# Optimization experiments

Hardware: AMD Instinct MI355X
Metric: run time of the kernel (lower is better)

Reference implementation:

```python
import jax, jax.numpy as jnp
import numpy as np

N, E, IN, HID, OUT, H, G = 50000, 800000, 128, 32, 32, 4, 64
NEG_SLOPE = 0.2


def setup_inputs() -> dict:
    key = jax.random.key(0)
    ks = jax.random.split(key, 12)
    p = lambda k, s: jax.random.normal(k, s, jnp.float32) * 0.1
    x = jax.random.normal(ks[0], (N, IN), jnp.float32)
    edge_index = jax.random.randint(ks[1], (2, E), 0, N, dtype=jnp.int64)
    batch = jnp.sort(jax.random.randint(ks[2], (N,), 0, G, dtype=jnp.int64))
    return {
        'x': x, 'edge_index': edge_index, 'batch': batch,
        'W1': p(ks[3], (IN, H * HID)),
        'att_src1': p(ks[4], (H, HID)), 'att_dst1': p(ks[5], (H, HID)),
        'b1': jnp.zeros((H * HID,), jnp.float32),
        'W2': p(ks[6], (H * HID, H * OUT)),
        'att_src2': p(ks[7], (H, OUT)), 'att_dst2': p(ks[8], (H, OUT)),
        'b2': jnp.zeros((H * OUT,), jnp.float32),
        'lin_w': p(ks[9], (H * OUT, 1)),
        'lin_b': jnp.zeros((1,), jnp.float32),
    }


def gat_conv(x, src, dst, W, a_src, a_dst, b, heads, ch):
    # x: [N, F_in]; src/dst: [E'] with self-loops already appended.
    n = x.shape[0]
    h = (x @ W).reshape(n, heads, ch)                      # [N, H, C]
    alpha_s = jnp.einsum('nhc,hc->nh', h, a_src)           # [N, H]
    alpha_d = jnp.einsum('nhc,hc->nh', h, a_dst)
    e = jax.nn.leaky_relu(alpha_s[src] + alpha_d[dst], NEG_SLOPE)  # [E', H]
    # segment softmax over destination neighborhoods
    m = jax.ops.segment_max(e, dst, num_segments=n)
    m = jnp.where(jnp.isfinite(m), m, 0.0)
    ex = jnp.exp(e - m[dst])
    s = jax.ops.segment_sum(ex, dst, num_segments=n)
    alpha = ex / (s[dst] + 1e-16)                          # [E', H]
    out = jax.ops.segment_sum(alpha[:, :, None] * h[src], dst, num_segments=n)
    return out.reshape(n, heads * ch) + b


def reference(x, edge_index, batch, W1, att_src1, att_dst1, b1,
              W2, att_src2, att_dst2, b2, lin_w, lin_b):
    # add self-loops (PyG GATConv default add_self_loops=True)
    loops = jnp.arange(N, dtype=edge_index.dtype)
    src = jnp.concatenate([edge_index[0], loops])
    dst = jnp.concatenate([edge_index[1], loops])

    h = jax.nn.elu(gat_conv(x, src, dst, W1, att_src1, att_dst1, b1, H, HID))
    h = gat_conv(h, src, dst, W2, att_src2, att_dst2, b2, H, OUT)  # [N, H*OUT]

    # global mean + max pool per graph
    counts = jax.ops.segment_sum(jnp.ones((N,), h.dtype), batch, num_segments=G)
    mean_p = jax.ops.segment_sum(h, batch, num_segments=G) / jnp.maximum(counts, 1.0)[:, None]
    max_p = jax.ops.segment_max(h, batch, num_segments=G)
    max_p = jnp.where(jnp.isfinite(max_p), max_p, 0.0)
    pooled = mean_p + max_p                                # [G, H*OUT]
    return pooled @ lin_w + lin_b                          # [G, 1]
```

## Files before the change

kernel.cpp:

```cpp
#include <hip/hip_runtime.h>
#include <hip/hip_bf16.h>
#include <hip/hip_fp16.h>
#include <math.h>

#define NEG_SLOPE 0.2f
#define BCAP 64
#define LAYER_W 18432

typedef _Float16 half8 __attribute__((ext_vector_type(8)));
typedef _Float16 half4v __attribute__((ext_vector_type(4)));
typedef float f32x4 __attribute__((ext_vector_type(4)));


__device__ __forceinline__ int lbound(const int* __restrict__ a, int n, int key) {
    int lo = 0, hi = n;
    while (lo < hi) {
        int mid = (lo + hi) >> 1;
        if (a[mid] < key) lo = mid + 1; else hi = mid;
    }
    return lo;
}

__device__ __forceinline__ unsigned encf(float f) {
    unsigned u = __float_as_uint(f);
    return (u & 0x80000000u) ? ~u : (u | 0x80000000u);
}
__device__ __forceinline__ float decf(unsigned u) {
    return (u & 0x80000000u) ? __uint_as_float(u & 0x7FFFFFFFu) : __uint_as_float(~u);
}


__global__ void prep_kernel(const float* __restrict__ W1, const float* __restrict__ W2,
                            const float* __restrict__ as1, const float* __restrict__ ad1,
                            const float* __restrict__ as2, const float* __restrict__ ad2,
                            _Float16* __restrict__ wt_hi, _Float16* __restrict__ wt_lo,
                            int* __restrict__ cnt, float* __restrict__ gsum,
                            unsigned* __restrict__ gmax, int n, int gtot) {
    int b = blockIdx.x;
    if (b < 72) {
        int lane = threadIdx.x;
        if (lane >= 64) return;
        int layer = b / 36;
        int rem = b % 36;
        int nt = rem >> 2;
        int kc = rem & 3;
        const float* W  = layer ? W2 : W1;
        const float* As = layer ? as2 : as1;
        const float* Ad = layer ? ad2 : ad1;
        int nn = lane & 15, q = lane >> 4;
        size_t base = (size_t)layer * LAYER_W + (size_t)((nt * 4 + kc) * 64 + lane) * 8;
        #pragma unroll
        for (int j = 0; j < 8; ++j) {
            int k = kc * 32 + q * 8 + j;
            float w = 0.f;
            if (nt < 8) {
                w = W[(size_t)k * 128 + nt * 16 + nn];
            } else if (nn < 4) {
                for (int c = 0; c < 32; ++c) w += W[(size_t)k * 128 + nn * 32 + c] * As[nn * 32 + c];
            } else if (nn < 8) {
                int hh = nn - 4;
                for (int c = 0; c < 32; ++c) w += W[(size_t)k * 128 + hh * 32 + c] * Ad[hh * 32 + c];
            }
            _Float16 hi = (_Float16)w;
            wt_hi[base + j] = hi;
            wt_lo[base + j] = (_Float16)(w - (float)hi);
        }
        return;
    }
    int i = (b - 72) * 256 + threadIdx.x;
    if (i < n) cnt[i] = 0;
    if (i < gtot) { gsum[i] = 0.f; gmax[i] = 0u; }
}


__global__ void build_kernel(const int* __restrict__ src, const int* __restrict__ dst,
                             int* __restrict__ cnt, unsigned short* __restrict__ col,
                             int E, int n) {
    int part  = blockIdx.x & 7;
    int chunk = blockIdx.x >> 3;
    int i = chunk * 256 + threadIdx.x;
    if (i >= E) return;
    int d = dst[i];
    int psz = (n + 7) >> 3;
    int lo = part * psz;
    if (d < lo || d >= lo + psz) return;
    int slot = atomicAdd(&cnt[d], 1);
    if (slot < BCAP - 1) col[(size_t)d * BCAP + slot] = (unsigned short)src[i];
}


template <bool A16>
__global__ __launch_bounds__(256) void gemm_attn_kernel(
        const void* __restrict__ Araw,
        const _Float16* __restrict__ wt_hi, const _Float16* __restrict__ wt_lo,
        _Float16* __restrict__ H16, float* __restrict__ as_, float* __restrict__ ad_,
        int M) {
    __shared__ _Float16 a_st[64][136];

    int tid = threadIdx.x;
    int m0 = blockIdx.x * 64;

    if (A16) {
        const _Float16* A = (const _Float16*)Araw;
        #pragma unroll
        for (int t = 0; t < 4; ++t) {
            int f = tid + t * 256;
            int r = f >> 4;
            int c8 = (f & 15) << 3;
            int gr = m0 + r; if (gr >= M) gr = M - 1;
            *(half8*)&a_st[r][c8] = *(const half8*)(A + (size_t)gr * 128 + c8);
        }
    } else {
        const float* A = (const float*)Araw;
        #pragma unroll
        for (int t = 0; t < 8; ++t) {
            int f = tid + t * 256;
            int r = f >> 5;
            int c4 = (f & 31) << 2;
            int gr = m0 + r; if (gr >= M) gr = M - 1;
            const float4 v = *(const float4*)(A + (size_t)gr * 128 + c4);
            half4v hi = { (_Float16)v.x, (_Float16)v.y, (_Float16)v.z, (_Float16)v.w };
            *(half4v*)&a_st[r][c4] = hi;
        }
    }
    __syncthreads();

    int w = tid >> 6;
    int lane = tid & 63;
    int cbase = lane & 15;
    int q = lane >> 4;
    int mrow = (w << 4) + cbase;

    f32x4 acc[9];
    #pragma unroll
    for (int nt = 0; nt < 9; ++nt) acc[nt] = (f32x4){0.f, 0.f, 0.f, 0.f};

    #pragma unroll
    for (int kc = 0; kc < 4; ++kc) {
        half8 ah = *(half8*)&a_st[mrow][kc * 32 + q * 8];
        #pragma unroll
        for (int nt = 0; nt < 9; ++nt) {
            const half8 bh = *(const half8*)(wt_hi + (size_t)((nt * 4 + kc) * 64 + lane) * 8);
            const half8 bl = *(const half8*)(wt_lo + (size_t)((nt * 4 + kc) * 64 + lane) * 8);
            acc[nt] = __builtin_amdgcn_mfma_f32_16x16x32_f16(ah, bh, acc[nt], 0, 0, 0);
            acc[nt] = __builtin_amdgcn_mfma_f32_16x16x32_f16(ah, bl, acc[nt], 0, 0, 0);
        }
    }

    #pragma unroll
    for (int nt = 0; nt < 8; ++nt) {
        int c = nt * 16 + cbase;
        #pragma unroll
        for (int i = 0; i < 4; ++i) {
            int gr = m0 + (w << 4) + (q << 2) + i;
            if (gr < M) H16[(size_t)gr * 128 + c] = (_Float16)acc[nt][i];
        }
    }
    if (cbase < 8) {
        #pragma unroll
        for (int i = 0; i < 4; ++i) {
            int gr = m0 + (w << 4) + (q << 2) + i;
            if (gr < M) {
                if (cbase < 4) as_[(size_t)gr * 4 + cbase]     = acc[8][i];
                else           ad_[(size_t)gr * 4 + cbase - 4] = acc[8][i];
            }
        }
    }
}


__global__ __launch_bounds__(256) void agg_kernel(
        const int* __restrict__ cnt, const unsigned short* __restrict__ col,
        const _Float16* __restrict__ h16, const float* __restrict__ as_,
        const float* __restrict__ ad_, const float* __restrict__ bias,
        _Float16* __restrict__ out16, int n, int elu) {
    __shared__ int   s_col[4][64];
    __shared__ float s_w[4][256];

    int wvb  = threadIdx.x >> 6;
    int lane = threadIdx.x & 63;
    int wv   = blockIdx.x * 4 + wvb;
    int valid = (wv < n);
    if (!valid) wv = n - 1;

    int degr = cnt[wv]; if (degr > BCAP - 1) degr = BCAP - 1;
    int deg = degr + 1;
    const unsigned short* crow = col + (size_t)wv * BCAP;
    const float4 adv = *(const float4*)(ad_ + (size_t)wv * 4);

    int q = lane >> 4;
    int r = lane & 15;
    int head = r >> 2;
    const _Float16* hrow = h16 + 8 * r;

    if (lane < deg) {
        int s = (lane == degr) ? wv : (int)crow[lane];
        const float4 av = *(const float4*)(as_ + (size_t)s * 4);
        float e0 = av.x + adv.x, e1 = av.y + adv.y;
        float e2 = av.z + adv.z, e3 = av.w + adv.w;
        float w0 = __expf(fmaxf(e0, NEG_SLOPE * e0));
        float w1 = __expf(fmaxf(e1, NEG_SLOPE * e1));
        float w2 = __expf(fmaxf(e2, NEG_SLOPE * e2));
        float w3 = __expf(fmaxf(e3, NEG_SLOPE * e3));
        s_col[wvb][lane] = s;
        *(float4*)&s_w[wvb][lane * 4] = make_float4(w0, w1, w2, w3);
    } else {
        s_col[wvb][lane] = 0;
        *(float4*)&s_w[wvb][lane * 4] = make_float4(0.f, 0.f, 0.f, 0.f);
    }
    __syncthreads();

    float lsum = 0.f;
    float acc[8];
    #pragma unroll
    for (int j = 0; j < 8; ++j) acc[j] = 0.f;

    for (int it = 0; it < deg; it += 16) {
        int ea = it + q;
        int eb = ea + 4;
        int ec = ea + 8;
        int ed = ea + 12;
        int sa = s_col[wvb][ea];
        int sb = s_col[wvb][eb];
        int sc = s_col[wvb][ec];
        int sd = s_col[wvb][ed];
        float wa = s_w[wvb][ea * 4 + head];
        float wb = s_w[wvb][eb * 4 + head];
        float wc = s_w[wvb][ec * 4 + head];
        float wd = s_w[wvb][ed * 4 + head];
        const half8 ha = *(const half8*)(hrow + (size_t)sa * 128);
        const half8 hb = *(const half8*)(hrow + (size_t)sb * 128);
        const half8 hc = *(const half8*)(hrow + (size_t)sc * 128);
        const half8 hd = *(const half8*)(hrow + (size_t)sd * 128);
        lsum += wa + wb + wc + wd;
        #pragma unroll
        for (int j = 0; j < 8; ++j)
            acc[j] += wa * (float)ha[j] + wb * (float)hb[j]
                    + wc * (float)hc[j] + wd * (float)hd[j];
    }

    #pragma unroll
    for (int j = 0; j < 8; ++j) {
        acc[j] += __shfl_xor(acc[j], 16, 64);
        acc[j] += __shfl_xor(acc[j], 32, 64);
    }
    lsum += __shfl_xor(lsum, 16, 64);
    lsum += __shfl_xor(lsum, 32, 64);

    if (lane < 16 && valid) {
        float inv = 1.f / (lsum + 1e-16f);
        const float4 bv0 = *(const float4*)(bias + 8 * r);
        const float4 bv1 = *(const float4*)(bias + 8 * r + 4);
        float o[8];
        o[0] = acc[0] * inv + bv0.x; o[1] = acc[1] * inv + bv0.y;
        o[2] = acc[2] * inv + bv0.z; o[3] = acc[3] * inv + bv0.w;
        o[4] = acc[4] * inv + bv1.x; o[5] = acc[5] * inv + bv1.y;
        o[6] = acc[6] * inv + bv1.z; o[7] = acc[7] * inv + bv1.w;
        if (elu) {
            #pragma unroll
            for (int j = 0; j < 8; ++j) o[j] = o[j] > 0.f ? o[j] : expm1f(o[j]);
        }
        half8 hv;
        #pragma unroll
        for (int j = 0; j < 8; ++j) hv[j] = (_Float16)o[j];
        *(half8*)(out16 + (size_t)wv * 128 + 8 * r) = hv;
    }
}


__global__ void pool1_kernel(const _Float16* __restrict__ h, const int* __restrict__ batch,
                             float* __restrict__ gsum, unsigned* __restrict__ gmax, int n) {
    int g = blockIdx.x >> 3;
    int p = blockIdx.x & 7;
    int c = threadIdx.x;
    int s = lbound(batch, n, g);
    int e = lbound(batch, n, g + 1);
    int len = e - s;
    int lo = s + (int)((long long)len * p / 8);
    int hi = s + (int)((long long)len * (p + 1) / 8);
    float sum = 0.f, mx = -INFINITY;
    for (int i = lo; i < hi; ++i) {
        float v = (float)h[(size_t)i * 128 + c];
        sum += v; mx = fmaxf(mx, v);
    }
    if (hi > lo) {
        atomicAdd(&gsum[g * 128 + c], sum);
        atomicMax(&gmax[g * 128 + c], encf(mx));
    }
}

__global__ void pool2_kernel(const float* __restrict__ gsum, const unsigned* __restrict__ gmax,
                             const int* __restrict__ batch, const float* __restrict__ lin_w,
                             const float* __restrict__ lin_b, float* __restrict__ out, int n) {
    int g = blockIdx.x;
    int c = threadIdx.x;
    int s = lbound(batch, n, g);
    int e = lbound(batch, n, g + 1);
    float cnt = fmaxf((float)(e - s), 1.0f);
    float mean = gsum[g * 128 + c] / cnt;
    float mx = decf(gmax[g * 128 + c]);
    if (!isfinite(mx)) mx = 0.f;
    float v = (mean + mx) * lin_w[c];
    __shared__ float red[128];
    red[c] = v;
    __syncthreads();
    for (int off = 64; off > 0; off >>= 1) {
        if (c < off) red[c] += red[c + off];
        __syncthreads();
    }
    if (c == 0) out[g] = red[0] + lin_b[0];
}


extern "C" void kernel_launch(void* const* d_in, const int* in_sizes, int n_in,
                              void* d_out, int out_size, void* d_ws, size_t ws_size,
                              hipStream_t stream) {
    const float* x    = (const float*)d_in[0];
    const int*   ei   = (const int*)d_in[1];
    const int*   batch= (const int*)d_in[2];
    const float* W1   = (const float*)d_in[3];
    const float* at_s1= (const float*)d_in[4];
    const float* at_d1= (const float*)d_in[5];
    const float* b1   = (const float*)d_in[6];
    const float* W2   = (const float*)d_in[7];
    const float* at_s2= (const float*)d_in[8];
    const float* at_d2= (const float*)d_in[9];
    const float* b2   = (const float*)d_in[10];
    const float* lw   = (const float*)d_in[11];
    const float* lb   = (const float*)d_in[12];
    float* out = (float*)d_out;

    const int N = in_sizes[0] / 128;
    const int E = in_sizes[1] / 2;
    const int G = out_size;

    char* p = (char*)d_ws;
    auto carve = [&](size_t bytes) -> void* {
        void* q = (void*)p;
        p += (bytes + 255) & ~(size_t)255;
        return q;
    };
    _Float16*       h16   = (_Float16*)carve((size_t)N * 128 * 2);
    _Float16*       a16   = (_Float16*)carve((size_t)N * 128 * 2);
    _Float16*       p16   = (_Float16*)carve((size_t)N * 128 * 2);
    float*          asb   = (float*)carve((size_t)N * 4 * 4);
    float*          adb   = (float*)carve((size_t)N * 4 * 4);
    int*            cnt   = (int*)carve((size_t)N * 4);
    unsigned short* col   = (unsigned short*)carve((size_t)N * BCAP * 2);
    float*          gsum  = (float*)carve((size_t)G * 128 * 4);
    unsigned*       gmax  = (unsigned*)carve((size_t)G * 128 * 4);
    _Float16*       wt_hi = (_Float16*)carve((size_t)2 * LAYER_W * 2);
    _Float16*       wt_lo = (_Float16*)carve((size_t)2 * LAYER_W * 2);

    const int* esrc = ei;
    const int* edst = ei + E;

    int initN = (N > G * 128) ? N : G * 128;
    prep_kernel<<<72 + (initN + 255) / 256, 256, 0, stream>>>(
        W1, W2, at_s1, at_d1, at_s2, at_d2, wt_hi, wt_lo, cnt, gsum, gmax, N, G * 128);

    const int nchunk = (E + 255) / 256;
    build_kernel<<<nchunk * 8, 256, 0, stream>>>(esrc, edst, cnt, col, E, N);

    gemm_attn_kernel<false><<<(N + 63) / 64, 256, 0, stream>>>(
        x, wt_hi, wt_lo, h16, asb, adb, N);
    agg_kernel<<<(N + 3) / 4, 256, 0, stream>>>(
        cnt, col, h16, asb, adb, b1, a16, N, 1);

    gemm_attn_kernel<true><<<(N + 63) / 64, 256, 0, stream>>>(
        a16, wt_hi + LAYER_W, wt_lo + LAYER_W, h16, asb, adb, N);
    agg_kernel<<<(N + 3) / 4, 256, 0, stream>>>(
        cnt, col, h16, asb, adb, b2, p16, N, 0);

    pool1_kernel<<<G * 8, 128, 0, stream>>>(p16, batch, gsum, gmax, N);
    pool2_kernel<<<G, 128, 0, stream>>>(gsum, gmax, batch, lw, lb, out, N);
}
```

Baseline: 280.9 us.

## Software-pipeline neighbor feature gathers in GAT aggregation, drop LDS column staging

The aggregation kernel now reads neighbor column indices straight from global memory as ushort4 per lane group and issues the first half8 feature gathers before the attention-weight computation. Later chunks are double-buffered so each gather overlaps the FMAs of the previous chunk. The shared column array goes away and the block-wide __syncthreads becomes a wave-local lgkmcnt wait, since each wave only reads its own LDS slice. Edge assignment moves from a strided to a contiguous mapping per lane group. Out-of-range slots point at the self row with zero weight, which adds redundant loads but removes the LDS round trip and the barrier.

```diff
diff --git a/kernel.cpp b/kernel.cpp
--- a/kernel.cpp
+++ b/kernel.cpp
@@ -174,7 +174,6 @@
         const _Float16* __restrict__ h16, const float* __restrict__ as_,
         const float* __restrict__ ad_, const float* __restrict__ bias,
         _Float16* __restrict__ out16, int n, int elu) {
-    __shared__ int   s_col[4][64];
     __shared__ float s_w[4][256];
 
     int wvb  = threadIdx.x >> 6;
@@ -186,13 +185,47 @@
     int degr = cnt[wv]; if (degr > BCAP - 1) degr = BCAP - 1;
     int deg = degr + 1;
     const unsigned short* crow = col + (size_t)wv * BCAP;
-    const float4 adv = *(const float4*)(ad_ + (size_t)wv * 4);
 
     int q = lane >> 4;
     int r = lane & 15;
     int head = r >> 2;
     const _Float16* hrow = h16 + 8 * r;
 
+    ushort4 cr0 = *(const ushort4*)(crow + 4 * q);
+    ushort4 cr1 = *(const ushort4*)(crow + 16 + 4 * q);
+
+#define GAT_ISSUE(CR, BASE, H0, H1, H2, H3)                                   \
+    do {                                                                      \
+        int e0_ = (BASE) + 4 * q;                                             \
+        int s0_ = (e0_ + 0 < degr) ? (int)(CR).x : wv;                        \
+        int s1_ = (e0_ + 1 < degr) ? (int)(CR).y : wv;                        \
+        int s2_ = (e0_ + 2 < degr) ? (int)(CR).z : wv;                        \
+        int s3_ = (e0_ + 3 < degr) ? (int)(CR).w : wv;                        \
+        H0 = *(const half8*)(hrow + (size_t)s0_ * 128);                       \
+        H1 = *(const half8*)(hrow + (size_t)s1_ * 128);                       \
+        H2 = *(const half8*)(hrow + (size_t)s2_ * 128);                       \
+        H3 = *(const half8*)(hrow + (size_t)s3_ * 128);                       \
+    } while (0)
+
+#define GAT_FMA(BASE, H0, H1, H2, H3)                                         \
+    do {                                                                      \
+        int e0_ = (BASE) + 4 * q;                                             \
+        float w0_ = s_w[wvb][(e0_ + 0) * 4 + head];                           \
+        float w1_ = s_w[wvb][(e0_ + 1) * 4 + head];                           \
+        float w2_ = s_w[wvb][(e0_ + 2) * 4 + head];                           \
+        float w3_ = s_w[wvb][(e0_ + 3) * 4 + head];                           \
+        lsum += w0_ + w1_ + w2_ + w3_;                                        \
+        _Pragma("unroll")                                                     \
+        for (int j = 0; j < 8; ++j)                                           \
+            acc[j] += w0_ * (float)H0[j] + w1_ * (float)H1[j]                 \
+                    + w2_ * (float)H2[j] + w3_ * (float)H3[j];                \
+    } while (0)
+
+    half8 ha0, ha1, ha2, ha3, hb0, hb1, hb2, hb3;
+
+    GAT_ISSUE(cr0, 0, ha0, ha1, ha2, ha3);
+
+    const float4 adv = *(const float4*)(ad_ + (size_t)wv * 4);
     if (lane < deg) {
         int s = (lane == degr) ? wv : (int)crow[lane];
         const float4 av = *(const float4*)(as_ + (size_t)s * 4);
@@ -202,42 +235,36 @@
         float w1 = __expf(fmaxf(e1, NEG_SLOPE * e1));
         float w2 = __expf(fmaxf(e2, NEG_SLOPE * e2));
         float w3 = __expf(fmaxf(e3, NEG_SLOPE * e3));
-        s_col[wvb][lane] = s;
         *(float4*)&s_w[wvb][lane * 4] = make_float4(w0, w1, w2, w3);
     } else {
-        s_col[wvb][lane] = 0;
         *(float4*)&s_w[wvb][lane * 4] = make_float4(0.f, 0.f, 0.f, 0.f);
     }
-    __syncthreads();
+    asm volatile("s_waitcnt lgkmcnt(0)" ::: "memory");
 
     float lsum = 0.f;
     float acc[8];
     #pragma unroll
     for (int j = 0; j < 8; ++j) acc[j] = 0.f;
 
-    for (int it = 0; it < deg; it += 16) {
-        int ea = it + q;
-        int eb = ea + 4;
-        int ec = ea + 8;
-        int ed = ea + 12;
-        int sa = s_col[wvb][ea];
-        int sb = s_col[wvb][eb];
-        int sc = s_col[wvb][ec];
-        int sd = s_col[wvb][ed];
-        float wa = s_w[wvb][ea * 4 + head];
-        float wb = s_w[wvb][eb * 4 + head];
-        float wc = s_w[wvb][ec * 4 + head];
-        float wd = s_w[wvb][ed * 4 + head];
-        const half8 ha = *(const half8*)(hrow + (size_t)sa * 128);
-        const half8 hb = *(const half8*)(hrow + (size_t)sb * 128);
-        const half8 hc = *(const half8*)(hrow + (size_t)sc * 128);
-        const half8 hd = *(const half8*)(hrow + (size_t)sd * 128);
-        lsum += wa + wb + wc + wd;
-        #pragma unroll
-        for (int j = 0; j < 8; ++j)
-            acc[j] += wa * (float)ha[j] + wb * (float)hb[j]
-                    + wc * (float)hc[j] + wd * (float)hd[j];
-    }
+    if (deg > 16) GAT_ISSUE(cr1, 16, hb0, hb1, hb2, hb3);
+    GAT_FMA(0, ha0, ha1, ha2, ha3);
+    if (deg > 16) {
+        if (deg > 32) {
+            ushort4 cr2 = *(const ushort4*)(crow + 32 + 4 * q);
+            GAT_ISSUE(cr2, 32, ha0, ha1, ha2, ha3);
+        }
+        GAT_FMA(16, hb0, hb1, hb2, hb3);
+        if (deg > 32) {
+            if (deg > 48) {
+                ushort4 cr3 = *(const ushort4*)(crow + 48 + 4 * q);
+                GAT_ISSUE(cr3, 48, hb0, hb1, hb2, hb3);
+            }
+            GAT_FMA(32, ha0, ha1, ha2, ha3);
+            if (deg > 48) GAT_FMA(48, hb0, hb1, hb2, hb3);
+        }
+    }
+#undef GAT_ISSUE
+#undef GAT_FMA
 
     #pragma unroll
     for (int j = 0; j < 8; ++j) {
```

Result: no change. 276.0 us (-1.7%).

## Store self-loops in CSR and prefetch first 32 neighbor rows before softmax

Applied to the files above, without the earlier changes.

Self-loop edges are now written into the neighbor table by the build kernel, and the column buffer is zeroed in the prep kernel. This lets the aggregation kernel issue loads for the first 32 neighbor feature rows right away, before it computes the attention weights, so the exp computation overlaps those gathers. The block-wide barrier is replaced with an lgkmcnt wait, the weight shared-memory layout becomes head-major for vector reads, and a loop over the remaining neighbors handles rare high-degree nodes. The costs are always gathering 32 rows (zero-padded to node 0) even for low-degree nodes, and extra zeroing and build work for the N self-loops.

```diff
diff --git a/kernel.cpp b/kernel.cpp
--- a/kernel.cpp
+++ b/kernel.cpp
@@ -35,7 +35,8 @@
                             const float* __restrict__ as2, const float* __restrict__ ad2,
                             _Float16* __restrict__ wt_hi, _Float16* __restrict__ wt_lo,
                             int* __restrict__ cnt, float* __restrict__ gsum,
-                            unsigned* __restrict__ gmax, int n, int gtot) {
+                            unsigned* __restrict__ gmax, unsigned short* __restrict__ col,
+                            int n, int gtot) {
     int b = blockIdx.x;
     if (b < 72) {
         int lane = threadIdx.x;
@@ -70,6 +71,7 @@
     int i = (b - 72) * 256 + threadIdx.x;
     if (i < n) cnt[i] = 0;
     if (i < gtot) { gsum[i] = 0.f; gmax[i] = 0u; }
+    if (i < n * 8) ((uint4*)col)[i] = make_uint4(0u, 0u, 0u, 0u);
 }
 
 
@@ -79,13 +81,16 @@
     int part  = blockIdx.x & 7;
     int chunk = blockIdx.x >> 3;
     int i = chunk * 256 + threadIdx.x;
-    if (i >= E) return;
-    int d = dst[i];
+    if (i >= E + n) return;
+    int d = (i < E) ? dst[i] : (i - E);
     int psz = (n + 7) >> 3;
     int lo = part * psz;
     if (d < lo || d >= lo + psz) return;
     int slot = atomicAdd(&cnt[d], 1);
-    if (slot < BCAP - 1) col[(size_t)d * BCAP + slot] = (unsigned short)src[i];
+    if (slot < BCAP) {
+        int s = (i < E) ? src[i] : d;
+        col[(size_t)d * BCAP + slot] = (unsigned short)s;
+    }
 }
 
 
@@ -174,8 +179,7 @@
         const _Float16* __restrict__ h16, const float* __restrict__ as_,
         const float* __restrict__ ad_, const float* __restrict__ bias,
         _Float16* __restrict__ out16, int n, int elu) {
-    __shared__ int   s_col[4][64];
-    __shared__ float s_w[4][256];
+    __shared__ float s_w[4][4][64];
 
     int wvb  = threadIdx.x >> 6;
     int lane = threadIdx.x & 63;
@@ -183,60 +187,69 @@
     int valid = (wv < n);
     if (!valid) wv = n - 1;
 
-    int degr = cnt[wv]; if (degr > BCAP - 1) degr = BCAP - 1;
-    int deg = degr + 1;
     const unsigned short* crow = col + (size_t)wv * BCAP;
-    const float4 adv = *(const float4*)(ad_ + (size_t)wv * 4);
-
     int q = lane >> 4;
     int r = lane & 15;
     int head = r >> 2;
-    const _Float16* hrow = h16 + 8 * r;
-
+    unsigned roff = (unsigned)r << 4;
+    const char* hb = (const char*)h16;
+
+    ushort4 cr0 = *(const ushort4*)(crow + 4 * q);
+    ushort4 cr1 = *(const ushort4*)(crow + 16 + 4 * q);
+    half8 ha0 = *(const half8*)(hb + (((unsigned)cr0.x << 8) | roff));
+    half8 ha1 = *(const half8*)(hb + (((unsigned)cr0.y << 8) | roff));
+    half8 ha2 = *(const half8*)(hb + (((unsigned)cr0.z << 8) | roff));
+    half8 ha3 = *(const half8*)(hb + (((unsigned)cr0.w << 8) | roff));
+    half8 hb0 = *(const half8*)(hb + (((unsigned)cr1.x << 8) | roff));
+    half8 hb1 = *(const half8*)(hb + (((unsigned)cr1.y << 8) | roff));
+    half8 hb2 = *(const half8*)(hb + (((unsigned)cr1.z << 8) | roff));
+    half8 hb3 = *(const half8*)(hb + (((unsigned)cr1.w << 8) | roff));
+
+    int deg = cnt[wv]; if (deg > BCAP) deg = BCAP;
+
+    const float4 adv = *(const float4*)(ad_ + (size_t)wv * 4);
+    float w0 = 0.f, w1 = 0.f, w2 = 0.f, w3 = 0.f;
     if (lane < deg) {
-        int s = (lane == degr) ? wv : (int)crow[lane];
+        int s = crow[lane];
         const float4 av = *(const float4*)(as_ + (size_t)s * 4);
         float e0 = av.x + adv.x, e1 = av.y + adv.y;
         float e2 = av.z + adv.z, e3 = av.w + adv.w;
-        float w0 = __expf(fmaxf(e0, NEG_SLOPE * e0));
-        float w1 = __expf(fmaxf(e1, NEG_SLOPE * e1));
-        float w2 = __expf(fmaxf(e2, NEG_SLOPE * e2));
-        float w3 = __expf(fmaxf(e3, NEG_SLOPE * e3));
-        s_col[wvb][lane] = s;
-        *(float4*)&s_w[wvb][lane * 4] = make_float4(w0, w1, w2, w3);
-    } else {
-        s_col[wvb][lane] = 0;
-        *(float4*)&s_w[wvb][lane * 4] = make_float4(0.f, 0.f, 0.f, 0.f);
-    }
-    __syncthreads();
-
-    float lsum = 0.f;
+        w0 = __expf(fmaxf(e0, NEG_SLOPE * e0));
+        w1 = __expf(fmaxf(e1, NEG_SLOPE * e1));
+        w2 = __expf(fmaxf(e2, NEG_SLOPE * e2));
+        w3 = __expf(fmaxf(e3, NEG_SLOPE * e3));
+    }
+    s_w[wvb][0][lane] = w0;
+    s_w[wvb][1][lane] = w1;
+    s_w[wvb][2][lane] = w2;
+    s_w[wvb][3][lane] = w3;
+    asm volatile("s_waitcnt lgkmcnt(0)" ::: "memory");
+
+    f32x4 wa = *(const f32x4*)&s_w[wvb][head][4 * q];
+    f32x4 wb = *(const f32x4*)&s_w[wvb][head][16 + 4 * q];
+    float lsum = (wa.x + wa.y + wa.z + wa.w) + (wb.x + wb.y + wb.z + wb.w);
     float acc[8];
     #pragma unroll
-    for (int j = 0; j < 8; ++j) acc[j] = 0.f;
-
-    for (int it = 0; it < deg; it += 16) {
-        int ea = it + q;
-        int eb = ea + 4;
-        int ec = ea + 8;
-        int ed = ea + 12;
-        int sa = s_col[wvb][ea];
-        int sb = s_col[wvb][eb];
-        int sc = s_col[wvb][ec];
-        int sd = s_col[wvb][ed];
-        float wa = s_w[wvb][ea * 4 + head];
-        float wb = s_w[wvb][eb * 4 + head];
-        float wc = s_w[wvb][ec * 4 + head];
-        float wd = s_w[wvb][ed * 4 + head];
-        const half8 ha = *(const half8*)(hrow + (size_t)sa * 128);
-        const half8 hb = *(const half8*)(hrow + (size_t)sb * 128);
-        const half8 hc = *(const half8*)(hrow + (size_t)sc * 128);
-        const half8 hd = *(const half8*)(hrow + (size_t)sd * 128);
-        lsum += wa + wb + wc + wd;
-        #pragma unroll
-        for (int j = 0; j < 8; ++j)
-            acc[j] += wa * (float)ha[j] + wb * (float)hb[j]
-                    + wc * (float)hc[j] + wd * (float)hd[j];
+    for (int j = 0; j < 8; ++j)
+        acc[j] = wa.x * (float)ha0[j] + wa.y * (float)ha1[j]
+               + wa.z * (float)ha2[j] + wa.w * (float)ha3[j]
+               + wb.x * (float)hb0[j] + wb.y * (float)hb1[j]
+               + wb.z * (float)hb2[j] + wb.w * (float)hb3[j];
+
+    if (__builtin_expect(deg > 32, 0)) {
+        for (int base = 32; base < deg; base += 16) {
+            ushort4 cr = *(const ushort4*)(crow + base + 4 * q);
+            half8 t0 = *(const half8*)(hb + (((unsigned)cr.x << 8) | roff));
+            half8 t1 = *(const half8*)(hb + (((unsigned)cr.y << 8) | roff));
+            half8 t2 = *(const half8*)(hb + (((unsigned)cr.z << 8) | roff));
+            half8 t3 = *(const half8*)(hb + (((unsigned)cr.w << 8) | roff));
+            f32x4 wt = *(const f32x4*)&s_w[wvb][head][base + 4 * q];
+            lsum += wt.x + wt.y + wt.z + wt.w;
+            #pragma unroll
+            for (int j = 0; j < 8; ++j)
+                acc[j] += wt.x * (float)t0[j] + wt.y * (float)t1[j]
+                        + wt.z * (float)t2[j] + wt.w * (float)t3[j];
+        }
     }
 
     #pragma unroll
@@ -355,11 +368,12 @@
     const int* esrc = ei;
     const int* edst = ei + E;
 
-    int initN = (N > G * 128) ? N : G * 128;
+    int initN = N * 8;
+    if (initN < G * 128) initN = G * 128;
     prep_kernel<<<72 + (initN + 255) / 256, 256, 0, stream>>>(
-        W1, W2, at_s1, at_d1, at_s2, at_d2, wt_hi, wt_lo, cnt, gsum, gmax, N, G * 128);
-
-    const int nchunk = (E + 255) / 256;
+        W1, W2, at_s1, at_d1, at_s2, at_d2, wt_hi, wt_lo, cnt, gsum, gmax, col, N, G * 128);
+
+    const int nchunk = (E + N + 255) / 256;
     build_kernel<<<nchunk * 8, 256, 0, stream>>>(esrc, edst, cnt, col, E, N);
 
     gemm_attn_kernel<false><<<(N + 63) / 64, 256, 0, stream>>>(
```

Measured after the change: 279.8 us. Within noise of the previous version (-0.4%).
